# Kernel optimization log

Hardware: AMD Instinct MI355X
Metric: run time of the kernel (lower is better)

## Reference

```python
import jax, jax.numpy as jnp
import numpy as np

B, N, D, R = 2, 256, 128, 32

def _sh_l1(r):
    # e3nn-style component-normalized l=1 spherical harmonics of unit vectors
    return jnp.sqrt(3.0) * r

def _sh_l2(r):
    x, y, z = r[..., 0], r[..., 1], r[..., 2]
    c = jnp.sqrt(15.0)
    return jnp.stack([
        c * x * y,
        c * y * z,
        0.5 * jnp.sqrt(5.0) * (3.0 * z * z - 1.0),  # x^2+y^2+z^2 = 1
        c * x * z,
        0.5 * c * (x * x - y * y),
    ], axis=-1)

def _radial(rbf, w1, b1, w2, b2):
    h = rbf @ w1 + b1
    return (h * jax.nn.sigmoid(h)) @ w2 + b2  # Linear -> SiLU -> Linear

def _layernorm(x, g, b, eps=1e-5):
    m = jnp.mean(x, axis=-1, keepdims=True)
    v = jnp.var(x, axis=-1, keepdims=True)
    return (x - m) * jax.lax.rsqrt(v + eps) * g + b

def setup_inputs() -> dict:
    key = jax.random.key(0)
    ks = iter(jax.random.split(key, 40))
    def nrm(shape, s=1.0):
        return jax.random.normal(next(ks), shape, dtype=jnp.float32) * s
    r_hat = nrm((B, N, N, 3))
    r_hat = r_hat / (jnp.linalg.norm(r_hat, axis=-1, keepdims=True) + 1e-9)
    inp = {
        'node_s': nrm((B, N, D)),
        'node_v': nrm((B, N, 3, D)),
        'node_t': nrm((B, N, 5, D)),
        'rbf': jax.random.uniform(next(ks), (B, N, N, R), dtype=jnp.float32),
        'r_hat': r_hat,
        'mask': jnp.ones((B, N, N), dtype=jnp.float32),
    }
    s1, s2 = 1.0 / np.sqrt(R), 1.0 / np.sqrt(D)
    for p in ('r0', 'r1', 'r2', 'r110'):
        inp[p + '_w1'] = nrm((R, D), s1)
        inp[p + '_b1'] = jnp.zeros((D,), jnp.float32)
        inp[p + '_w2'] = nrm((D, D), s2)
        inp[p + '_b2'] = jnp.zeros((D,), jnp.float32)
    inp['src_w'] = nrm((D, D), s2)
    inp['ln_g'] = jnp.ones((D,), jnp.float32)
    inp['ln_b'] = jnp.zeros((D,), jnp.float32)
    inp['out_w'] = nrm((D, D), s2)
    inp['out_b'] = jnp.zeros((D,), jnp.float32)
    inp['v_scale'] = jnp.ones((D,), jnp.float32)
    inp['t_scale'] = jnp.ones((D,), jnp.float32)
    return inp

def reference(node_s, node_v, node_t, rbf, r_hat, mask,
              r0_w1, r0_b1, r0_w2, r0_b2,
              r1_w1, r1_b1, r1_w2, r1_b2,
              r2_w1, r2_b1, r2_w2, r2_b2,
              r110_w1, r110_b1, r110_w2, r110_b2,
              src_w, ln_g, ln_b, out_w, out_b, v_scale, t_scale):
    h = node_s @ src_w                               # (B,N,D)
    h_j = h[:, None, :, :] * mask[..., None]         # (B,N,N,D): h_j[b,i,j]=h[b,j]*mask[b,i,j]
    Y1 = _sh_l1(r_hat)                               # (B,N,N,3)
    Y2 = _sh_l2(r_hat)                               # (B,N,N,5)

    msg_s = jnp.sum(h_j * _radial(rbf, r0_w1, r0_b1, r0_w2, r0_b2), axis=2)  # (B,N,D)
    delta_v = jnp.einsum('bijd,bijc->bicd',
                         h_j * _radial(rbf, r1_w1, r1_b1, r1_w2, r1_b2), Y1) * v_scale
    delta_t = jnp.einsum('bijd,bijc->bicd',
                         h_j * _radial(rbf, r2_w1, r2_b1, r2_w2, r2_b2), Y2) * t_scale

    # v_j[b,i,j] = node_v[b,i] (per the torch unsqueeze(2).expand)
    dot_vY1 = jnp.einsum('bicd,bijc->bijd', node_v, Y1)                      # (B,N,N,D)
    msg_s_from_v = jnp.sum(dot_vY1 * _radial(rbf, r110_w1, r110_b1, r110_w2, r110_b2)
                           * mask[..., None], axis=2)                        # (B,N,D)

    delta_s = _layernorm(msg_s + msg_s_from_v, ln_g, ln_b) @ out_w + out_b
    return (delta_s, delta_v, delta_t)
```

## Files before the change

kernel.cpp:

```cpp
#include <hip/hip_runtime.h>

#define Bb 2
#define Nn 256
#define Dd 128
#define Rr 32

typedef unsigned short u16;
typedef unsigned int   u32;
typedef __attribute__((ext_vector_type(8))) short bf16x8;
typedef __attribute__((ext_vector_type(4))) short bf16x4;
typedef __attribute__((ext_vector_type(4))) float f32x4;
typedef __attribute__((ext_vector_type(2))) u32   u32x2;

__device__ __forceinline__ short f2bfs(float f){
  u32 u = __float_as_uint(f);
  u += 0x7FFFu + ((u >> 16) & 1u);
  return (short)(u >> 16);
}
__device__ __forceinline__ u16 f2bf(float f){
  u32 u = __float_as_uint(f);
  u += 0x7FFFu + ((u >> 16) & 1u);
  return (u16)(u >> 16);
}

__global__ __launch_bounds__(128) void hproj_kernel(
    const float* __restrict__ node_s, const float* __restrict__ src_w,
    float* __restrict__ h_out){
  __shared__ float s_row[Dd];
  const int bi = blockIdx.x, d = threadIdx.x;
  s_row[d] = node_s[(size_t)bi*Dd + d];
  __syncthreads();
  float acc = 0.f;
  #pragma unroll 8
  for (int k=0;k<Dd;k++) acc += s_row[k]*src_w[k*Dd + d];
  h_out[(size_t)bi*Dd + d] = acc;
}

__global__ __launch_bounds__(256,2) void se3_mfma3(
    const float* __restrict__ node_v,
    const float* __restrict__ rbf,
    const float* __restrict__ r_hat,
    const float* __restrict__ maskp,
    const float* __restrict__ r0w1, const float* __restrict__ r0b1,
    const float* __restrict__ r0w2, const float* __restrict__ r0b2,
    const float* __restrict__ r1w1, const float* __restrict__ r1b1,
    const float* __restrict__ r1w2, const float* __restrict__ r1b2,
    const float* __restrict__ r2w1, const float* __restrict__ r2b1,
    const float* __restrict__ r2w2, const float* __restrict__ r2b2,
    const float* __restrict__ r3w1, const float* __restrict__ r3b1,
    const float* __restrict__ r3w2, const float* __restrict__ r3b2,
    const float* __restrict__ ln_g, const float* __restrict__ ln_b,
    const float* __restrict__ out_w, const float* __restrict__ out_b,
    const float* __restrict__ v_scale, const float* __restrict__ t_scale,
    const float* __restrict__ h_ws,
    float* __restrict__ out_s, float* __restrict__ out_v, float* __restrict__ out_t)
{
  __shared__ u16   s_rbf[Nn*36];
  __shared__ u16   s_hid[64*136];
  __shared__ u16   s_YT[10*264];
  __shared__ u16   s_Y1r[3*264];
  __shared__ u16   s_G[4*32*72];
  __shared__ float s_msg[Dd];
  __shared__ float s_xn[Dd];
  __shared__ float s_part[2*Dd];
  __shared__ float s_mv[2];

  const int tid  = threadIdx.x;
  const int bi   = blockIdx.x;
  const int b    = bi >> 8;
  const int lane = tid & 63;
  const int w    = tid >> 6;
  const int q    = lane >> 4;
  const int cc   = lane & 15;
  const int dbase= w*32;

  {
    int j = tid;
    size_t pidx = (size_t)bi*Nn + j;
    float mk = maskp[pidx];
    float x = r_hat[pidx*3+0];
    float y = r_hat[pidx*3+1];
    float z = r_hat[pidx*3+2];
    const float SQ3=1.7320508075688772f;
    const float C15=3.8729833462074170f;
    const float C5H=1.1180339887498949f;
    float y1a=SQ3*x, y1b=SQ3*y, y1c=SQ3*z;
    s_YT[0*264+j]=f2bf(mk);
    s_YT[1*264+j]=f2bf(y1a*mk);
    s_YT[2*264+j]=f2bf(y1b*mk);
    s_YT[3*264+j]=f2bf(y1c*mk);
    s_YT[4*264+j]=f2bf(C15*x*y*mk);
    s_YT[5*264+j]=f2bf(C15*y*z*mk);
    s_YT[6*264+j]=f2bf(C5H*(3.f*z*z-1.f)*mk);
    s_YT[7*264+j]=f2bf(C15*x*z*mk);
    s_YT[8*264+j]=f2bf(0.5f*C15*(x*x-y*y)*mk);
    s_YT[9*264+j]=f2bf(mk);
    s_Y1r[0*264+j]=f2bf(y1a);
    s_Y1r[1*264+j]=f2bf(y1b);
    s_Y1r[2*264+j]=f2bf(y1c);
  }

  const float* rbf_blk = rbf + (size_t)bi*Nn*Rr;
  const float* hb      = h_ws + (size_t)b*Nn*Dd;

  for (int idx=tid; idx<Nn*Rr; idx+=256){
    int j = idx >> 5, r = idx & 31;
    s_rbf[j*36 + r] = f2bf(rbf_blk[idx]);
  }

  bf16x8 vBf[2];
  {
    const float* nv = node_v + (size_t)bi*3*Dd;
    #pragma unroll
    for (int nt=0;nt<2;nt++){
      int dd = dbase+nt*16+cc;
      bf16x8 t = {0,0,0,0,0,0,0,0};
      if (q==0){
        t[0]=f2bfs(nv[0*Dd+dd]);
        t[1]=f2bfs(nv[1*Dd+dd]);
        t[2]=f2bfs(nv[2*Dd+dd]);
      }
      vBf[nt]=t;
    }
  }

  const f32x4 zf = {0.f,0.f,0.f,0.f};
  f32x4 accred[2] = {zf, zf};

  #pragma unroll 1
  for (int p=0;p<4;p++){
    const float* W1p = (p==0)?r0w1:(p==1)?r1w1:(p==2)?r2w1:r3w1;
    const float* B1p = (p==0)?r0b1:(p==1)?r1b1:(p==2)?r2b1:r3b1;
    const float* W2p = (p==0)?r0w2:(p==1)?r1w2:(p==2)?r2w2:r3w2;
    const float* B2p = (p==0)?r0b2:(p==1)?r1b2:(p==2)?r2b2:r3b2;
    const int lo = (p==0)?0:(p==1)?1:(p==2)?4:9;
    const int hi = (p==0)?0:(p==1)?3:(p==2)?8:9;
    const u32 gmask = (cc>=lo && cc<=hi) ? 0xFFFFFFFFu : 0u;
    const u16* ytrow = &s_YT[(cc<10?cc:9)*264];

    bf16x8 w1f[2];
    bf16x8 w2f[2][4];
    float  b1v[2], b2v[2];
    #pragma unroll
    for (int nt=0;nt<2;nt++){
      int dd = dbase+nt*16+cc;
      b1v[nt]=B1p[dd];
      b2v[nt]=B2p[dd];
      #pragma unroll
      for (int jj=0;jj<8;jj++)
        w1f[nt][jj] = f2bfs(W1p[(q*8+jj)*Dd + dd]);
      #pragma unroll
      for (int ks=0;ks<4;ks++){
        #pragma unroll
        for (int jj=0;jj<8;jj++)
          w2f[nt][ks][jj] = f2bfs(W2p[(ks*32+q*8+jj)*Dd + dd]);
      }
    }

    #pragma unroll 1
    for (int ch=0; ch<4; ch++){
      __syncthreads();
      #pragma unroll
      for (int m=0;m<4;m++){
        const u16* ap = &s_rbf[(ch*64 + m*16 + cc)*36 + q*8];
        bf16x4 lo4 = *(const bf16x4*)ap;
        bf16x4 hi4 = *(const bf16x4*)(ap+4);
        bf16x8 raf = {lo4[0],lo4[1],lo4[2],lo4[3],hi4[0],hi4[1],hi4[2],hi4[3]};
        #pragma unroll
        for (int nt=0;nt<2;nt++){
          f32x4 hc = __builtin_amdgcn_mfma_f32_16x16x32_bf16(raf, w1f[nt], zf, 0,0,0);
          #pragma unroll
          for (int r=0;r<4;r++){
            float x  = hc[r] + b1v[nt];
            float e  = __expf(-x);
            float s  = x*__builtin_amdgcn_rcpf(1.f+e);
            s_hid[(m*16+q*4+r)*136 + dbase + nt*16 + cc] = f2bf(s);
          }
        }
      }
      __syncthreads();
      #pragma unroll
      for (int m=0;m<4;m++){
        bf16x8 af[4];
        #pragma unroll
        for (int ks=0;ks<4;ks++)
          af[ks] = *(const bf16x8*)&s_hid[(m*16+cc)*136 + ks*32 + q*8];

        f32x4 dotC[2];
        if (p==3){
          bf16x8 aY = {0,0,0,0,0,0,0,0};
          if (q==0){
            int j = ch*64 + m*16 + cc;
            aY[0]=(short)s_Y1r[0*264+j];
            aY[1]=(short)s_Y1r[1*264+j];
            aY[2]=(short)s_Y1r[2*264+j];
          }
          #pragma unroll
          for (int nt=0;nt<2;nt++)
            dotC[nt] = __builtin_amdgcn_mfma_f32_16x16x32_bf16(aY, vBf[nt], zf, 0,0,0);
        }

        #pragma unroll
        for (int nt=0;nt<2;nt++){
          f32x4 c2 = zf;
          #pragma unroll
          for (int ks=0;ks<4;ks++)
            c2 = __builtin_amdgcn_mfma_f32_16x16x32_bf16(af[ks], w2f[nt][ks], c2, 0,0,0);
          int dd = dbase+nt*16+cc;
          u16 g4[4];
          if (p<3){
            const float* hp = hb + (size_t)(ch*64 + m*16 + q*4)*Dd + dd;
            #pragma unroll
            for (int r=0;r<4;r++)
              g4[r] = f2bf((c2[r]+b2v[nt]) * hp[(size_t)r*Dd]);
          } else {
            #pragma unroll
            for (int r=0;r<4;r++)
              g4[r] = f2bf((c2[r]+b2v[nt]) * dotC[nt][r]);
          }
          u32x2 pk = { (u32)g4[0] | ((u32)g4[1]<<16),
                       (u32)g4[2] | ((u32)g4[3]<<16) };
          *(u32x2*)&s_G[(w*32 + nt*16 + cc)*72 + m*16 + q*4] = pk;
        }
      }
      #pragma unroll
      for (int ks2=0;ks2<2;ks2++){
        bf16x8 aR = *(const bf16x8*)(ytrow + ch*64 + ks2*32 + q*8);
        u32* arp = (u32*)&aR;
        arp[0]&=gmask; arp[1]&=gmask; arp[2]&=gmask; arp[3]&=gmask;
        #pragma unroll
        for (int nt=0;nt<2;nt++){
          bf16x8 bG = *(const bf16x8*)&s_G[(w*32 + nt*16 + cc)*72 + ks2*32 + q*8];
          accred[nt] = __builtin_amdgcn_mfma_f32_16x16x32_bf16(aR, bG, accred[nt], 0,0,0);
        }
      }
    }
  }

  #pragma unroll
  for (int nt=0;nt<2;nt++){
    int d = dbase + nt*16 + cc;
    #pragma unroll
    for (int r=0;r<4;r++){
      int rw = q*4 + r;
      float val = accred[nt][r];
      if (rw==0)      s_msg[d] = val;
      else if (rw<=3) out_v[(size_t)bi*3*Dd + (size_t)(rw-1)*Dd + d] = val*v_scale[d];
      else if (rw<=8) out_t[(size_t)bi*5*Dd + (size_t)(rw-4)*Dd + d] = val*t_scale[d];
      else if (rw==9) s_xn[d] = val;
    }
  }
  __syncthreads();

  if (tid < 64){
    float a0=s_msg[tid]+s_xn[tid], a1=s_msg[tid+64]+s_xn[tid+64];
    float s1=a0+a1, s2=a0*a0+a1*a1;
    #pragma unroll
    for (int off=1;off<64;off<<=1){
      s1 += __shfl_xor(s1,off);
      s2 += __shfl_xor(s2,off);
    }
    if (tid==0){
      float m   = s1*(1.f/Dd);
      float var = fmaxf(s2*(1.f/Dd) - m*m, 0.f);
      s_mv[0]=m;
      s_mv[1]=rsqrtf(var+1e-5f);
    }
  }
  __syncthreads();
  if (tid < Dd){
    float msg = s_msg[tid]+s_xn[tid];
    s_xn[tid] = (msg - s_mv[0])*s_mv[1]*ln_g[tid] + ln_b[tid];
  }
  __syncthreads();

  {
    int dp = tid & 127, seg = tid >> 7;
    float pa = 0.f;
    #pragma unroll 8
    for (int k=seg*64;k<seg*64+64;k++)
      pa += s_xn[k]*out_w[k*Dd+dp];
    s_part[seg*Dd+dp]=pa;
  }
  __syncthreads();
  if (tid < Dd)
    out_s[(size_t)bi*Dd+tid] = s_part[tid]+s_part[Dd+tid]+out_b[tid];
}

extern "C" void kernel_launch(void* const* d_in, const int* in_sizes, int n_in,
                              void* d_out, int out_size, void* d_ws, size_t ws_size,
                              hipStream_t stream) {
  const float* node_s = (const float*)d_in[0];
  const float* node_v = (const float*)d_in[1];
  const float* rbf    = (const float*)d_in[3];
  const float* r_hat  = (const float*)d_in[4];
  const float* maskp  = (const float*)d_in[5];
  const float* r0w1=(const float*)d_in[6],  *r0b1=(const float*)d_in[7];
  const float* r0w2=(const float*)d_in[8],  *r0b2=(const float*)d_in[9];
  const float* r1w1=(const float*)d_in[10], *r1b1=(const float*)d_in[11];
  const float* r1w2=(const float*)d_in[12], *r1b2=(const float*)d_in[13];
  const float* r2w1=(const float*)d_in[14], *r2b1=(const float*)d_in[15];
  const float* r2w2=(const float*)d_in[16], *r2b2=(const float*)d_in[17];
  const float* r3w1=(const float*)d_in[18], *r3b1=(const float*)d_in[19];
  const float* r3w2=(const float*)d_in[20], *r3b2=(const float*)d_in[21];
  const float* src_w  =(const float*)d_in[22];
  const float* ln_g   =(const float*)d_in[23];
  const float* ln_b   =(const float*)d_in[24];
  const float* out_w  =(const float*)d_in[25];
  const float* out_b  =(const float*)d_in[26];
  const float* v_scale=(const float*)d_in[27];
  const float* t_scale=(const float*)d_in[28];

  float* h_ws = (float*)d_ws;
  float* out_s = (float*)d_out;
  float* out_v = out_s + (size_t)Bb*Nn*Dd;
  float* out_t = out_v + (size_t)Bb*Nn*3*Dd;

  hproj_kernel<<<dim3(Bb*Nn), dim3(Dd), 0, stream>>>(node_s, src_w, h_ws);
  se3_mfma3<<<dim3(Bb*Nn), dim3(256), 0, stream>>>(
      node_v, rbf, r_hat, maskp,
      r0w1,r0b1,r0w2,r0b2, r1w1,r1b1,r1w2,r1b2,
      r2w1,r2b1,r2w2,r2b2, r3w1,r3b1,r3w2,r3b2,
      ln_g, ln_b, out_w, out_b, v_scale, t_scale,
      h_ws, out_s, out_v, out_t);
}
```

Before: 197.1 us.

## Drop shared rbf staging, transpose h for vector loads, raise occupancy

Removes the shared-memory copy of the rbf block and instead reads rbf straight from global memory inside the chunk loop, converting to bf16 on the fly. The first MFMA swaps its operands so each lane produces four consecutive hidden features, which allows a packed 8-byte shared store. The h projection is written transposed so the gating step can fetch four consecutive j values with one vector load. Freeing the rbf LDS and raising launch bounds to three blocks per CU are meant to increase occupancy, at the cost of reloading rbf from global memory once for each of the four radial passes.

```diff
diff --git a/kernel.cpp b/kernel.cpp
--- a/kernel.cpp
+++ b/kernel.cpp
@@ -25,18 +25,19 @@
 
 __global__ __launch_bounds__(128) void hproj_kernel(
     const float* __restrict__ node_s, const float* __restrict__ src_w,
-    float* __restrict__ h_out){
+    float* __restrict__ hT_out){
   __shared__ float s_row[Dd];
   const int bi = blockIdx.x, d = threadIdx.x;
+  const int b = bi >> 8, i = bi & 255;
   s_row[d] = node_s[(size_t)bi*Dd + d];
   __syncthreads();
   float acc = 0.f;
   #pragma unroll 8
   for (int k=0;k<Dd;k++) acc += s_row[k]*src_w[k*Dd + d];
-  h_out[(size_t)bi*Dd + d] = acc;
-}
-
-__global__ __launch_bounds__(256,2) void se3_mfma3(
+  hT_out[((size_t)b*Dd + d)*Nn + i] = acc;
+}
+
+__global__ __launch_bounds__(256,3) void se3_mfma4(
     const float* __restrict__ node_v,
     const float* __restrict__ rbf,
     const float* __restrict__ r_hat,
@@ -52,10 +53,9 @@
     const float* __restrict__ ln_g, const float* __restrict__ ln_b,
     const float* __restrict__ out_w, const float* __restrict__ out_b,
     const float* __restrict__ v_scale, const float* __restrict__ t_scale,
-    const float* __restrict__ h_ws,
+    const float* __restrict__ hT,
     float* __restrict__ out_s, float* __restrict__ out_v, float* __restrict__ out_t)
 {
-  __shared__ u16   s_rbf[Nn*36];
   __shared__ u16   s_hid[64*136];
   __shared__ u16   s_YT[10*264];
   __shared__ u16   s_Y1r[3*264];
@@ -101,12 +101,6 @@
   }
 
   const float* rbf_blk = rbf + (size_t)bi*Nn*Rr;
-  const float* hb      = h_ws + (size_t)b*Nn*Dd;
-
-  for (int idx=tid; idx<Nn*Rr; idx+=256){
-    int j = idx >> 5, r = idx & 31;
-    s_rbf[j*36 + r] = f2bf(rbf_blk[idx]);
-  }
 
   bf16x8 vBf[2];
   {
@@ -140,20 +134,21 @@
 
     bf16x8 w1f[2];
     bf16x8 w2f[2][4];
-    float  b1v[2], b2v[2];
+    f32x4  b1q[2];
+    float  b2v[2];
     #pragma unroll
-    for (int nt=0;nt<2;nt++){
-      int dd = dbase+nt*16+cc;
-      b1v[nt]=B1p[dd];
-      b2v[nt]=B2p[dd];
+    for (int mt=0;mt<2;mt++){
+      int dd = dbase+mt*16+cc;
+      b1q[mt] = *(const f32x4*)(B1p + dbase + mt*16 + q*4);
+      b2v[mt] = B2p[dd];
       #pragma unroll
       for (int jj=0;jj<8;jj++)
-        w1f[nt][jj] = f2bfs(W1p[(q*8+jj)*Dd + dd]);
+        w1f[mt][jj] = f2bfs(W1p[(q*8+jj)*Dd + dd]);
       #pragma unroll
       for (int ks=0;ks<4;ks++){
         #pragma unroll
         for (int jj=0;jj<8;jj++)
-          w2f[nt][ks][jj] = f2bfs(W2p[(ks*32+q*8+jj)*Dd + dd]);
+          w2f[mt][ks][jj] = f2bfs(W2p[(ks*32+q*8+jj)*Dd + dd]);
       }
     }
 
@@ -161,21 +156,25 @@
     for (int ch=0; ch<4; ch++){
       __syncthreads();
       #pragma unroll
-      for (int m=0;m<4;m++){
-        const u16* ap = &s_rbf[(ch*64 + m*16 + cc)*36 + q*8];
-        bf16x4 lo4 = *(const bf16x4*)ap;
-        bf16x4 hi4 = *(const bf16x4*)(ap+4);
-        bf16x8 raf = {lo4[0],lo4[1],lo4[2],lo4[3],hi4[0],hi4[1],hi4[2],hi4[3]};
-        #pragma unroll
-        for (int nt=0;nt<2;nt++){
-          f32x4 hc = __builtin_amdgcn_mfma_f32_16x16x32_bf16(raf, w1f[nt], zf, 0,0,0);
+      for (int jt=0;jt<4;jt++){
+        const float* rp = rbf_blk + (size_t)(ch*64 + jt*16 + cc)*Rr + q*8;
+        f32x4 ra0 = *(const f32x4*)rp;
+        f32x4 ra1 = *(const f32x4*)(rp+4);
+        bf16x8 raf = {f2bfs(ra0[0]),f2bfs(ra0[1]),f2bfs(ra0[2]),f2bfs(ra0[3]),
+                      f2bfs(ra1[0]),f2bfs(ra1[1]),f2bfs(ra1[2]),f2bfs(ra1[3])};
+        #pragma unroll
+        for (int mt=0;mt<2;mt++){
+          f32x4 hc = __builtin_amdgcn_mfma_f32_16x16x32_bf16(w1f[mt], raf, zf, 0,0,0);
+          u16 g4[4];
           #pragma unroll
           for (int r=0;r<4;r++){
-            float x  = hc[r] + b1v[nt];
+            float x  = hc[r] + b1q[mt][r];
             float e  = __expf(-x);
-            float s  = x*__builtin_amdgcn_rcpf(1.f+e);
-            s_hid[(m*16+q*4+r)*136 + dbase + nt*16 + cc] = f2bf(s);
+            g4[r] = f2bf(x*__builtin_amdgcn_rcpf(1.f+e));
           }
+          u32x2 pk = { (u32)g4[0] | ((u32)g4[1]<<16),
+                       (u32)g4[2] | ((u32)g4[3]<<16) };
+          *(u32x2*)&s_hid[(jt*16+cc)*136 + dbase + mt*16 + q*4] = pk;
         }
       }
       __syncthreads();
@@ -209,10 +208,10 @@
           int dd = dbase+nt*16+cc;
           u16 g4[4];
           if (p<3){
-            const float* hp = hb + (size_t)(ch*64 + m*16 + q*4)*Dd + dd;
+            f32x4 h4 = *(const f32x4*)(hT + ((size_t)(b*Dd) + dd)*Nn + ch*64 + m*16 + q*4);
             #pragma unroll
             for (int r=0;r<4;r++)
-              g4[r] = f2bf((c2[r]+b2v[nt]) * hp[(size_t)r*Dd]);
+              g4[r] = f2bf((c2[r]+b2v[nt]) * h4[r]);
           } else {
             #pragma unroll
             for (int r=0;r<4;r++)
@@ -311,16 +310,16 @@
   const float* v_scale=(const float*)d_in[27];
   const float* t_scale=(const float*)d_in[28];
 
-  float* h_ws = (float*)d_ws;
+  float* hT = (float*)d_ws;
   float* out_s = (float*)d_out;
   float* out_v = out_s + (size_t)Bb*Nn*Dd;
   float* out_t = out_v + (size_t)Bb*Nn*3*Dd;
 
-  hproj_kernel<<<dim3(Bb*Nn), dim3(Dd), 0, stream>>>(node_s, src_w, h_ws);
-  se3_mfma3<<<dim3(Bb*Nn), dim3(256), 0, stream>>>(
+  hproj_kernel<<<dim3(Bb*Nn), dim3(Dd), 0, stream>>>(node_s, src_w, hT);
+  se3_mfma4<<<dim3(Bb*Nn), dim3(256), 0, stream>>>(
       node_v, rbf, r_hat, maskp,
       r0w1,r0b1,r0w2,r0b2, r1w1,r1b1,r1w2,r1b2,
       r2w1,r2b1,r2w2,r2b2, r3w1,r3b1,r3w2,r3b2,
       ln_g, ln_b, out_w, out_b, v_scale, t_scale,
-      h_ws, out_s, out_v, out_t);
-}
+      hT, out_s, out_v, out_t);
+}
```

Measured after the change: 230.8 us. +17.1%, slower.
